# Kernel optimization log

Measured on AMD Instinct MI355X. Metric: run time of the kernel, lower is better.

## Reference

```python
import jax, jax.numpy as jnp
import numpy as np

N, D, H, C, E, I, L, B = 16000, 128, 2, 128, 256000, 512, 2, 64
NTYPES = 10


def setup_inputs() -> dict:
    key = jax.random.key(0)
    ks = jax.random.split(key, 20)
    s = 0.05
    inp = {
        'x': jax.random.normal(ks[0], (N, D), jnp.float32),
        'hetro_emb': jax.random.normal(ks[1], (NTYPES, D), jnp.float32) * s,
        'Wq': jax.random.normal(ks[2], (D, H * C), jnp.float32) * s,
        'bq': jnp.zeros((H * C,), jnp.float32),
        'Wk': jax.random.normal(ks[3], (D, H * C), jnp.float32) * s,
        'bk': jnp.zeros((H * C,), jnp.float32),
        'Wv': jax.random.normal(ks[4], (D, H * C), jnp.float32) * s,
        'bv': jnp.zeros((H * C,), jnp.float32),
        'We': jax.random.normal(ks[5], (D, H * C), jnp.float32) * s,
        'Wskip': jax.random.normal(ks[6], (D, C), jnp.float32) * s,
        'bskip': jnp.zeros((C,), jnp.float32),
        'ln_gamma': jnp.ones((L, D), jnp.float32),
        'ln_beta': jnp.zeros((L, D), jnp.float32),
        'ffn_w1': jax.random.normal(ks[7], (L, D, I), jnp.float32) * s,
        'ffn_b1': jnp.zeros((L, I), jnp.float32),
        'ffn_w2': jax.random.normal(ks[8], (L, I, D), jnp.float32) * s,
        'ffn_b2': jnp.zeros((L, D), jnp.float32),
        'edge_index': jax.random.randint(ks[9], (2, E), 0, N, jnp.int64),
        'edge_type': jax.random.randint(ks[10], (E,), 0, NTYPES, jnp.int64),
        'mask_idx': jax.random.randint(ks[11], (B,), 0, N, jnp.int64),
    }
    return inp


def _layer_norm(h, gamma, beta, eps=1e-6):
    mu = h.mean(-1, keepdims=True)
    var = ((h - mu) ** 2).mean(-1, keepdims=True)
    return (h - mu) * jax.lax.rsqrt(var + eps) * gamma + beta


def reference(x, hetro_emb, Wq, bq, Wk, bk, Wv, bv, We, Wskip, bskip,
              ln_gamma, ln_beta, ffn_w1, ffn_b1, ffn_w2, ffn_b2,
              edge_index, edge_type, mask_idx):
    src, dst = edge_index[0], edge_index[1]  # messages flow src(j) -> dst(i)
    edge_attr_raw = hetro_emb[edge_type]     # [E, D], computed once outside the layer loop
    scale = 1.0 / jnp.sqrt(jnp.asarray(C, x.dtype))

    h = x
    pre = h
    for l in range(L):
        # shared GRANConv weights across layers (same module appended n_gcn_layer times)
        q = (h @ Wq + bq).reshape(-1, H, C)
        k = (h @ Wk + bk).reshape(-1, H, C)
        v = (h @ Wv + bv).reshape(-1, H, C)
        eproj = (edge_attr_raw @ We).reshape(-1, H, C)  # [E, H, C]
        kj = k[src] + eproj                              # [E, H, C]
        logits = (q[dst] * kj).sum(-1) * scale           # [E, H]
        # segment softmax over destination nodes
        m = jax.ops.segment_max(logits, dst, num_segments=N)  # [N, H]
        a = jnp.exp(logits - m[dst])
        ssum = jax.ops.segment_sum(a, dst, num_segments=N)
        alpha = a / (ssum[dst] + 1e-16)                  # [E, H]
        msg = (v[src] + eproj) * alpha[..., None]        # [E, H, C]
        agg = jax.ops.segment_sum(msg, dst, num_segments=N)  # [N, H, C]
        out = agg.mean(1) + (h @ Wskip + bskip)          # concat=False -> head mean; root skip
        # residual + LN + FFN (no activation between the two FFN linears)
        hres = out + pre
        hln = _layer_norm(hres, ln_gamma[l], ln_beta[l])
        h = (hln @ ffn_w1[l] + ffn_b1[l]) @ ffn_w2[l] + ffn_b2[l]
        pre = h

    return h[mask_idx]  # [B, D]
```

## Files before the change

### kernel.cpp

```cpp
#include <hip/hip_runtime.h>
#include <hip/hip_bf16.h>
#include <math.h>

#define DD 128
#define QW 896
#define CAP 96

typedef _Float16 f16x8 __attribute__((ext_vector_type(8)));
typedef _Float16 f16x4 __attribute__((ext_vector_type(4)));
typedef float f32x4 __attribute__((ext_vector_type(4)));

__global__ __launch_bounds__(256) void count_kernel(const int* __restrict__ edst,
                                                    int* __restrict__ counts, int E) {
  int e = blockIdx.x * 256 + threadIdx.x;
  if (e < E) atomicAdd(&counts[edst[e]], 1);
}

__global__ __launch_bounds__(1024) void scan_kernel(const int* __restrict__ counts,
                                                    int* __restrict__ offs,
                                                    int* __restrict__ cursor, int Nn) {
  __shared__ int part[1024];
  int tid = threadIdx.x;
  int chunk = (Nn + 1023) >> 10;
  int b = tid * chunk, e = min(b + chunk, Nn);
  int s = 0;
  for (int j = b; j < e; ++j) s += counts[j];
  part[tid] = s;
  __syncthreads();
  for (int d = 1; d < 1024; d <<= 1) {
    int v = (tid >= d) ? part[tid - d] : 0;
    __syncthreads();
    part[tid] += v;
    __syncthreads();
  }
  int excl = tid ? part[tid - 1] : 0;
  for (int j = b; j < e; ++j) { offs[j] = excl; cursor[j] = excl; excl += counts[j]; }
  if (tid == 1023) offs[Nn] = part[1023];
}

__global__ __launch_bounds__(256) void scatter_kernel(const int* __restrict__ edst,
                                                      const int* __restrict__ esrc,
                                                      const int* __restrict__ etyp,
                                                      int* __restrict__ cursor,
                                                      unsigned* __restrict__ epk, int E) {
  int e = blockIdx.x * 256 + threadIdx.x;
  if (e < E) {
    int pos = atomicAdd(&cursor[edst[e]], 1);
    epk[pos] = (unsigned)esrc[e] | ((unsigned)etyp[e] << 18);
  }
}

__global__ __launch_bounds__(256) void precompute1(
    const float* __restrict__ Wq, const float* __restrict__ Wk,
    const float* __restrict__ Wv, const float* __restrict__ Wsk,
    const float* __restrict__ bq, const float* __restrict__ bk,
    const float* __restrict__ bv, const float* __restrict__ bsk,
    const float* __restrict__ hemb, const float* __restrict__ We,
    const float* __restrict__ x,
    const float* __restrict__ fw1, const float* __restrict__ fb1,
    const float* __restrict__ fw2, const float* __restrict__ fb2,
    _Float16* __restrict__ WcatT, float* __restrict__ Wcat, float* __restrict__ bcat,
    _Float16* __restrict__ epth, _Float16* __restrict__ xh,
    float* __restrict__ Wf, float* __restrict__ bfv, int Nn) {
  int t = blockIdx.x * 256 + threadIdx.x;
  if (t < 114688) {
    int n = t >> 7, k = t & 127;
    float v;
    if (n < 256) v = Wq[k * 256 + n];
    else if (n < 512) v = Wk[k * 256 + (n - 256)];
    else if (n < 768) v = Wv[k * 256 + (n - 512)];
    else v = Wsk[k * 128 + (n - 768)];
    WcatT[t] = (_Float16)v;
    Wcat[k * 896 + n] = v;
    return;
  }
  t -= 114688;
  if (t < 896) {
    float v;
    if (t < 256) v = bq[t];
    else if (t < 512) v = bk[t - 256];
    else if (t < 768) v = bv[t - 512];
    else v = bsk[t - 768];
    bcat[t] = v;
    return;
  }
  t -= 896;
  if (t < 2560) {
    int ty = t >> 8, col = t & 255;
    float s = 0.f;
#pragma unroll 4
    for (int c = 0; c < 128; ++c) s = fmaf(hemb[ty * 128 + c], We[c * 256 + col], s);
    epth[t] = (_Float16)s;
    return;
  }
  t -= 2560;
  if (t < Nn * 16) {
    float4 v0 = *reinterpret_cast<const float4*>(x + (size_t)t * 8);
    float4 v1 = *reinterpret_cast<const float4*>(x + (size_t)t * 8 + 4);
    f16x8 o;
    o[0] = (_Float16)v0.x; o[1] = (_Float16)v0.y; o[2] = (_Float16)v0.z; o[3] = (_Float16)v0.w;
    o[4] = (_Float16)v1.x; o[5] = (_Float16)v1.y; o[6] = (_Float16)v1.z; o[7] = (_Float16)v1.w;
    *reinterpret_cast<f16x8*>(xh + (size_t)t * 8) = o;
    return;
  }
  t -= Nn * 16;
  if (t < 32768) {
    int l = t >> 14, rem = t & 16383;
    int i2 = rem >> 7, j = rem & 127;
    const float* a = fw1 + (size_t)l * 65536 + i2 * 512;
    const float* b2 = fw2 + (size_t)l * 65536 + j;
    float s = 0.f;
#pragma unroll 4
    for (int k = 0; k < 512; ++k) s = fmaf(a[k], b2[k * 128], s);
    Wf[t] = s;
    return;
  }
  t -= 32768;
  if (t < 256) {
    int l = t >> 7, j = t & 127;
    const float* b1 = fb1 + l * 512;
    const float* w2 = fw2 + (size_t)l * 65536 + j;
    float s = fb2[l * 128 + j];
#pragma unroll 4
    for (int k = 0; k < 512; ++k) s = fmaf(b1[k], w2[k * 128], s);
    bfv[t] = s;
  }
}

__global__ __launch_bounds__(256) void precompute2(
    const float* __restrict__ Wf, const float* __restrict__ Wcat,
    const float* __restrict__ bfv, const float* __restrict__ bcat,
    _Float16* __restrict__ BtMid, float* __restrict__ bmid) {
  int t = blockIdx.x * 256 + threadIdx.x;
  if (t < 131072) {
    int k = t >> 10, n = t & 1023;
    float v;
    if (n < 128) v = Wf[k * 128 + n];
    else {
      const float* wr = Wf + k * 128;
      const float* wc = Wcat + (n - 128);
      float s = 0.f;
#pragma unroll 4
      for (int c = 0; c < 128; ++c) s = fmaf(wr[c], wc[c * 896], s);
      v = s;
    }
    BtMid[(size_t)n * 128 + k] = (_Float16)v;
    return;
  }
  t -= 131072;
  if (t < 1024) {
    float v;
    if (t < 128) v = bfv[t];
    else {
      const float* wc = Wcat + (t - 128);
      float s = bcat[t - 128];
#pragma unroll 4
      for (int c = 0; c < 128; ++c) s = fmaf(bfv[c], wc[c * 896], s);
      v = s;
    }
    bmid[t] = v;
  }
}

__global__ __launch_bounds__(256) void gemm_tn_f16(const _Float16* __restrict__ A,
                                                   const _Float16* __restrict__ Bt,
                                                   const float* __restrict__ bias,
                                                   float* __restrict__ Cf, int NF,
                                                   _Float16* __restrict__ Ch, int choff, int ldh,
                                                   int M, int N, int K) {
  const int tid = threadIdx.x;
  const int wid = tid >> 6, lane = tid & 63;
  const int wr = wid >> 1, wc = wid & 1;
  const int il = lane & 15, g = lane >> 4;
  const int row0 = blockIdx.x * 128 + wr * 64;
  const int col0 = blockIdx.y * 128 + wc * 64;
  const _Float16* Ap = A + (size_t)(row0 + il) * K + 8 * g;
  const _Float16* Bp = Bt + (size_t)(col0 + il) * K + 8 * g;
  f32x4 acc[4][4];
#pragma unroll
  for (int a = 0; a < 4; ++a)
#pragma unroll
    for (int b = 0; b < 4; ++b) acc[a][b] = (f32x4){0.f, 0.f, 0.f, 0.f};
  for (int k0 = 0; k0 < K; k0 += 32) {
    f16x8 af[4], bf[4];
#pragma unroll
    for (int f = 0; f < 4; ++f) {
      af[f] = *reinterpret_cast<const f16x8*>(Ap + (size_t)(f * 16) * K + k0);
      bf[f] = *reinterpret_cast<const f16x8*>(Bp + (size_t)(f * 16) * K + k0);
    }
#pragma unroll
    for (int fi = 0; fi < 4; ++fi)
#pragma unroll
      for (int fj = 0; fj < 4; ++fj)
        acc[fi][fj] = __builtin_amdgcn_mfma_f32_16x16x32_f16(af[fi], bf[fj], acc[fi][fj], 0, 0, 0);
  }
#pragma unroll
  for (int fj = 0; fj < 4; ++fj) {
    const int col = col0 + fj * 16 + il;
    const float b = bias[col];
#pragma unroll
    for (int fi = 0; fi < 4; ++fi) {
#pragma unroll
      for (int i = 0; i < 4; ++i) {
        const int row = row0 + fi * 16 + g * 4 + i;
        const float v = acc[fi][fj][i] + b;
        if (Cf && col < NF) Cf[(size_t)row * NF + col] = v;
        if (Ch && col >= choff) Ch[(size_t)row * ldh + (col - choff)] = (_Float16)v;
      }
    }
  }
}

__global__ __launch_bounds__(256) void node_attn_ln_kernel(
    const _Float16* __restrict__ QKVSh, const _Float16* __restrict__ epth,
    const float* __restrict__ hpre,
    const int* __restrict__ offs, const unsigned* __restrict__ epk,
    const float* __restrict__ gamma, const float* __restrict__ beta,
    _Float16* __restrict__ hlnh, int Nn) {
  __shared__ float sl0[4][CAP], sl1[4][CAP];
  __shared__ unsigned spk[4][CAP];
  __shared__ __align__(16) _Float16 elds[2560];
  const int tid = threadIdx.x;
  for (int t = tid; t < 1280; t += 256)
    reinterpret_cast<unsigned*>(elds)[t] = reinterpret_cast<const unsigned*>(epth)[t];
  __syncthreads();
  const int w = tid >> 6, lane = tid & 63;
  const int i = blockIdx.x * 4 + w;
  const int sub = lane >> 5;
  const int r = lane & 31;
  const int half = r >> 4;
  const int co = r << 3;
  const float scale = 0.08838834764831845f;
  float q[8];
  {
    f16x8 qv = *reinterpret_cast<const f16x8*>(QKVSh + (size_t)i * QW + co);
#pragma unroll
    for (int t = 0; t < 8; ++t) q[t] = (float)qv[t];
  }
  float m0 = -1e30f, m1 = -1e30f, s0 = 0.f, s1 = 0.f;
  float acc[8] = {0.f};
  const int ebeg = offs[i], eend = offs[i + 1];
  for (int cs = ebeg; cs < eend; cs += CAP) {
    const int cnt = min(CAP, eend - cs);
    for (int j = lane; j < cnt; j += 64) spk[w][j] = epk[cs + j];
    __threadfence_block();
    {
      int jj = (sub < cnt) ? sub : (cnt - 1);
      unsigned pk = spk[w][jj];
      f16x8 kv = *reinterpret_cast<const f16x8*>(QKVSh + (size_t)(pk & 0x3FFFF) * QW + 256 + co);
      f16x8 ev = *reinterpret_cast<const f16x8*>(elds + ((pk >> 18) << 8) + co);
      for (int j = 0; j < cnt; j += 2) {
        f16x8 kc = kv, ec = ev;
        const bool valid = (j + sub) < cnt;
        int jn = j + 2 + sub; if (jn > cnt - 1) jn = cnt - 1;
        pk = spk[w][jn];
        kv = *reinterpret_cast<const f16x8*>(QKVSh + (size_t)(pk & 0x3FFFF) * QW + 256 + co);
        ev = *reinterpret_cast<const f16x8*>(elds + ((pk >> 18) << 8) + co);
        float d = 0.f;
#pragma unroll
        for (int t = 0; t < 8; ++t) d = fmaf(q[t], (float)kc[t] + (float)ec[t], d);
        d += __shfl_xor(d, 1); d += __shfl_xor(d, 2);
        d += __shfl_xor(d, 4); d += __shfl_xor(d, 8);
        d *= scale;
        if (valid) {
          if (r == 0) sl0[w][j + sub] = d;
          if (r == 16) sl1[w][j + sub] = d;
        }
      }
    }
    __threadfence_block();
    float lm0 = -1e30f, lm1 = -1e30f;
    for (int j = lane; j < cnt; j += 64) {
      lm0 = fmaxf(lm0, sl0[w][j]); lm1 = fmaxf(lm1, sl1[w][j]);
    }
#pragma unroll
    for (int o = 32; o; o >>= 1) {
      lm0 = fmaxf(lm0, __shfl_xor(lm0, o)); lm1 = fmaxf(lm1, __shfl_xor(lm1, o));
    }
    const float nm0 = fmaxf(m0, lm0), nm1 = fmaxf(m1, lm1);
    const float r0 = __expf(m0 - nm0), r1 = __expf(m1 - nm1);
    const float rme = half ? r1 : r0;
    s0 *= r0; s1 *= r1;
#pragma unroll
    for (int t = 0; t < 8; ++t) acc[t] *= rme;
    m0 = nm0; m1 = nm1;
    float ls0 = 0.f, ls1 = 0.f;
    for (int j = lane; j < cnt; j += 64) {
      float e0 = __expf(sl0[w][j] - m0);
      float e1 = __expf(sl1[w][j] - m1);
      sl0[w][j] = e0; sl1[w][j] = e1;
      ls0 += e0; ls1 += e1;
    }
#pragma unroll
    for (int o = 32; o; o >>= 1) { ls0 += __shfl_xor(ls0, o); ls1 += __shfl_xor(ls1, o); }
    s0 += ls0; s1 += ls1;
    __threadfence_block();
    {
      int jj = (sub < cnt) ? sub : (cnt - 1);
      unsigned pk = spk[w][jj];
      f16x8 vv = *reinterpret_cast<const f16x8*>(QKVSh + (size_t)(pk & 0x3FFFF) * QW + 512 + co);
      f16x8 ev = *reinterpret_cast<const f16x8*>(elds + ((pk >> 18) << 8) + co);
      for (int j = 0; j < cnt; j += 2) {
        f16x8 vc = vv, ec = ev;
        const int jcur = j + sub;
        float wj = 0.f;
        if (jcur < cnt) wj = half ? sl1[w][jcur] : sl0[w][jcur];
        int jn = j + 2 + sub; if (jn > cnt - 1) jn = cnt - 1;
        pk = spk[w][jn];
        vv = *reinterpret_cast<const f16x8*>(QKVSh + (size_t)(pk & 0x3FFFF) * QW + 512 + co);
        ev = *reinterpret_cast<const f16x8*>(elds + ((pk >> 18) << 8) + co);
#pragma unroll
        for (int t = 0; t < 8; ++t) acc[t] = fmaf((float)vc[t] + (float)ec[t], wj, acc[t]);
      }
    }
  }
  const float inv0 = 1.f / (s0 + 1e-16f), inv1 = 1.f / (s1 + 1e-16f);
  const float invme = half ? inv1 : inv0;
  float g[8];
#pragma unroll
  for (int t = 0; t < 8; ++t) {
    float a = acc[t] + __shfl_xor(acc[t], 32);
    a *= invme;
    g[t] = 0.5f * (a + __shfl_xor(a, 16));
  }
  const int cm = (r & 15) << 3;
  f16x8 sk = *reinterpret_cast<const f16x8*>(QKVSh + (size_t)i * QW + 768 + cm);
  float4 p0 = *reinterpret_cast<const float4*>(hpre + (size_t)i * DD + cm);
  float4 p1 = *reinterpret_cast<const float4*>(hpre + (size_t)i * DD + cm + 4);
  float xv[8];
  xv[0] = g[0] + (float)sk[0] + p0.x; xv[1] = g[1] + (float)sk[1] + p0.y;
  xv[2] = g[2] + (float)sk[2] + p0.z; xv[3] = g[3] + (float)sk[3] + p0.w;
  xv[4] = g[4] + (float)sk[4] + p1.x; xv[5] = g[5] + (float)sk[5] + p1.y;
  xv[6] = g[6] + (float)sk[6] + p1.z; xv[7] = g[7] + (float)sk[7] + p1.w;
  float sm = 0.f;
#pragma unroll
  for (int t = 0; t < 8; ++t) sm += xv[t];
  sm += __shfl_xor(sm, 1); sm += __shfl_xor(sm, 2);
  sm += __shfl_xor(sm, 4); sm += __shfl_xor(sm, 8);
  const float mu = sm * (1.f / 128.f);
  float vvs = 0.f;
  float dx[8];
#pragma unroll
  for (int t = 0; t < 8; ++t) { dx[t] = xv[t] - mu; vvs += dx[t] * dx[t]; }
  vvs += __shfl_xor(vvs, 1); vvs += __shfl_xor(vvs, 2);
  vvs += __shfl_xor(vvs, 4); vvs += __shfl_xor(vvs, 8);
  const float rstd = rsqrtf(vvs * (1.f / 128.f) + 1e-6f);
  if (lane < 16) {
    float4 gm0 = *reinterpret_cast<const float4*>(gamma + cm);
    float4 gm1 = *reinterpret_cast<const float4*>(gamma + cm + 4);
    float4 bt0 = *reinterpret_cast<const float4*>(beta + cm);
    float4 bt1 = *reinterpret_cast<const float4*>(beta + cm + 4);
    f16x8 o;
    o[0] = (_Float16)(dx[0] * rstd * gm0.x + bt0.x);
    o[1] = (_Float16)(dx[1] * rstd * gm0.y + bt0.y);
    o[2] = (_Float16)(dx[2] * rstd * gm0.z + bt0.z);
    o[3] = (_Float16)(dx[3] * rstd * gm0.w + bt0.w);
    o[4] = (_Float16)(dx[4] * rstd * gm1.x + bt1.x);
    o[5] = (_Float16)(dx[5] * rstd * gm1.y + bt1.y);
    o[6] = (_Float16)(dx[6] * rstd * gm1.z + bt1.z);
    o[7] = (_Float16)(dx[7] * rstd * gm1.w + bt1.w);
    *reinterpret_cast<f16x8*>(hlnh + (size_t)i * DD + cm) = o;
  }
}

__global__ __launch_bounds__(128) void final_kernel(const _Float16* __restrict__ hlnh1,
                                                    const float* __restrict__ Wf,
                                                    const float* __restrict__ bfv,
                                                    const int* __restrict__ midx,
                                                    float* __restrict__ out) {
  __shared__ float rowv[128];
  const int b = blockIdx.x, j = threadIdx.x;
  const int row = midx[b];
  rowv[j] = (float)hlnh1[(size_t)row * DD + j];
  __syncthreads();
  const float* w1 = Wf + 16384 + j;
  float s = bfv[128 + j];
#pragma unroll 4
  for (int c = 0; c < 128; ++c) s = fmaf(rowv[c], w1[c * 128], s);
  out[b * DD + j] = s;
}

extern "C" void kernel_launch(void* const* d_in, const int* in_sizes, int n_in,
                              void* d_out, int out_size, void* d_ws, size_t ws_size,
                              hipStream_t stream) {
  const float* x    = (const float*)d_in[0];
  const float* hemb = (const float*)d_in[1];
  const float* Wq   = (const float*)d_in[2];
  const float* bq   = (const float*)d_in[3];
  const float* Wk   = (const float*)d_in[4];
  const float* bk   = (const float*)d_in[5];
  const float* Wv   = (const float*)d_in[6];
  const float* bv   = (const float*)d_in[7];
  const float* We   = (const float*)d_in[8];
  const float* Wsk  = (const float*)d_in[9];
  const float* bsk  = (const float*)d_in[10];
  const float* lng  = (const float*)d_in[11];
  const float* lnb  = (const float*)d_in[12];
  const float* fw1  = (const float*)d_in[13];
  const float* fb1  = (const float*)d_in[14];
  const float* fw2  = (const float*)d_in[15];
  const float* fb2  = (const float*)d_in[16];
  const int* eidx   = (const int*)d_in[17];
  const int* etyp   = (const int*)d_in[18];
  const int* midx   = (const int*)d_in[19];

  const int Nn = in_sizes[0] / DD;
  const int E = in_sizes[18];

  const int* esrc = eidx;
  const int* edst = eidx + E;

  char* p = (char*)d_ws;
  auto alloc = [&](size_t bytes) -> void* {
    void* r = (void*)p;
    p += (bytes + 255) & ~(size_t)255;
    return r;
  };
  _Float16* QKVSh = (_Float16*)alloc((size_t)Nn * QW * 2);
  _Float16* xh    = (_Float16*)alloc((size_t)Nn * DD * 2);
  _Float16* hln0  = (_Float16*)alloc((size_t)Nn * DD * 2);
  _Float16* hln1  = (_Float16*)alloc((size_t)Nn * DD * 2);
  float*    h1    = (float*)alloc((size_t)Nn * DD * 4);
  _Float16* WcatT = (_Float16*)alloc((size_t)QW * DD * 2);
  float*    Wcat  = (float*)alloc((size_t)DD * QW * 4);
  float*    bcat  = (float*)alloc(QW * 4);
  _Float16* epth  = (_Float16*)alloc(2560 * 2);
  float*    Wf    = (float*)alloc(2 * 128 * 128 * 4);
  float*    bfv   = (float*)alloc(256 * 4);
  _Float16* BtMid = (_Float16*)alloc((size_t)1024 * 128 * 2);
  float*    bmid  = (float*)alloc(1024 * 4);
  int* counts = (int*)alloc((size_t)Nn * 4);
  int* offs   = (int*)alloc((size_t)(Nn + 1) * 4);
  int* cursor = (int*)alloc((size_t)Nn * 4);
  unsigned* epk = (unsigned*)alloc((size_t)E * 4);

  hipMemsetAsync(counts, 0, (size_t)Nn * sizeof(int), stream);
  count_kernel<<<(E + 255) / 256, 256, 0, stream>>>(edst, counts, E);
  scan_kernel<<<1, 1024, 0, stream>>>(counts, offs, cursor, Nn);
  scatter_kernel<<<(E + 255) / 256, 256, 0, stream>>>(edst, esrc, etyp, cursor, epk, E);

  const int p1_threads = 114688 + 896 + 2560 + Nn * 16 + 32768 + 256;
  precompute1<<<(p1_threads + 255) / 256, 256, 0, stream>>>(
      Wq, Wk, Wv, Wsk, bq, bk, bv, bsk, hemb, We, x, fw1, fb1, fw2, fb2,
      WcatT, Wcat, bcat, epth, xh, Wf, bfv, Nn);
  precompute2<<<(131072 + 1024 + 255) / 256, 256, 0, stream>>>(Wf, Wcat, bfv, bcat, BtMid, bmid);

  dim3 g1(Nn / 128, QW / 128);
  gemm_tn_f16<<<g1, 256, 0, stream>>>(xh, WcatT, bcat, nullptr, 0, QKVSh, 0, QW, Nn, QW, DD);
  node_attn_ln_kernel<<<Nn / 4, 256, 0, stream>>>(QKVSh, epth, x, offs, epk,
                                                  lng, lnb, hln0, Nn);
  dim3 g2(Nn / 128, 1024 / 128);
  gemm_tn_f16<<<g2, 256, 0, stream>>>(hln0, BtMid, bmid, h1, 128, QKVSh, 128, QW, Nn, 1024, DD);
  node_attn_ln_kernel<<<Nn / 4, 256, 0, stream>>>(QKVSh, epth, h1, offs, epk,
                                                  lng + DD, lnb + DD, hln1, Nn);
  final_kernel<<<64, 128, 0, stream>>>(hln1, Wf, bfv, midx, (float*)d_out);
}
```

Before: 280.9 us.

## Compute fused FFN weights via MFMA GEMMs and restructure edge attention

```diff
diff --git a/kernel.cpp b/kernel.cpp
--- a/kernel.cpp
+++ b/kernel.cpp
@@ -4,11 +4,20 @@
 
 #define DD 128
 #define QW 896
-#define CAP 96
+#define CAP 128
 
 typedef _Float16 f16x8 __attribute__((ext_vector_type(8)));
 typedef _Float16 f16x4 __attribute__((ext_vector_type(4)));
+typedef _Float16 f16x2 __attribute__((ext_vector_type(2)));
 typedef float f32x4 __attribute__((ext_vector_type(4)));
+
+__device__ __forceinline__ float fdot2f(f16x2 a, f16x2 b, float c) {
+#if __has_builtin(__builtin_amdgcn_fdot2)
+  return __builtin_amdgcn_fdot2(a, b, c, false);
+#else
+  return fmaf((float)a[0], (float)b[0], fmaf((float)a[1], (float)b[1], c));
+#endif
+}
 
 __global__ __launch_bounds__(256) void count_kernel(const int* __restrict__ edst,
                                                     int* __restrict__ counts, int E) {
@@ -50,7 +59,7 @@
   }
 }
 
-__global__ __launch_bounds__(256) void precompute1(
+__global__ __launch_bounds__(256) void pp_cast(
     const float* __restrict__ Wq, const float* __restrict__ Wk,
     const float* __restrict__ Wv, const float* __restrict__ Wsk,
     const float* __restrict__ bq, const float* __restrict__ bk,
@@ -61,8 +70,38 @@
     const float* __restrict__ fw2, const float* __restrict__ fb2,
     _Float16* __restrict__ WcatT, float* __restrict__ Wcat, float* __restrict__ bcat,
     _Float16* __restrict__ epth, _Float16* __restrict__ xh,
-    float* __restrict__ Wf, float* __restrict__ bfv, int Nn) {
+    _Float16* __restrict__ fw1h, _Float16* __restrict__ fw2Th,
+    float* __restrict__ bfv, float* __restrict__ bzero, int Nn) {
   int t = blockIdx.x * 256 + threadIdx.x;
+  if (t < 256) {
+    int l = t >> 7, j = t & 127;
+    const float* b1 = fb1 + l * 512;
+    const float* w2 = fw2 + (size_t)l * 65536 + j;
+    float s0 = fb2[l * 128 + j], s1 = 0.f, s2 = 0.f, s3 = 0.f;
+    for (int k = 0; k < 512; k += 4) {
+      s0 = fmaf(b1[k], w2[(size_t)k * 128], s0);
+      s1 = fmaf(b1[k + 1], w2[(size_t)(k + 1) * 128], s1);
+      s2 = fmaf(b1[k + 2], w2[(size_t)(k + 2) * 128], s2);
+      s3 = fmaf(b1[k + 3], w2[(size_t)(k + 3) * 128], s3);
+    }
+    bfv[t] = ((s0 + s1) + (s2 + s3));
+    return;
+  }
+  t -= 256;
+  if (t < 2560) {
+    int ty = t >> 8, col = t & 255;
+    float s0 = 0.f, s1 = 0.f, s2 = 0.f, s3 = 0.f;
+    const float* hr = hemb + ty * 128;
+    for (int c = 0; c < 128; c += 4) {
+      s0 = fmaf(hr[c], We[c * 256 + col], s0);
+      s1 = fmaf(hr[c + 1], We[(c + 1) * 256 + col], s1);
+      s2 = fmaf(hr[c + 2], We[(c + 2) * 256 + col], s2);
+      s3 = fmaf(hr[c + 3], We[(c + 3) * 256 + col], s3);
+    }
+    epth[t] = (_Float16)((s0 + s1) + (s2 + s3));
+    return;
+  }
+  t -= 2560;
   if (t < 114688) {
     int n = t >> 7, k = t & 127;
     float v;
@@ -85,15 +124,25 @@
     return;
   }
   t -= 896;
-  if (t < 2560) {
-    int ty = t >> 8, col = t & 255;
-    float s = 0.f;
-#pragma unroll 4
-    for (int c = 0; c < 128; ++c) s = fmaf(hemb[ty * 128 + c], We[c * 256 + col], s);
-    epth[t] = (_Float16)s;
-    return;
-  }
-  t -= 2560;
+  if (t < 1024) { bzero[t] = 0.f; return; }
+  t -= 1024;
+  if (t < 16384) {
+    float4 v0 = *reinterpret_cast<const float4*>(fw1 + (size_t)t * 8);
+    float4 v1 = *reinterpret_cast<const float4*>(fw1 + (size_t)t * 8 + 4);
+    f16x8 o;
+    o[0] = (_Float16)v0.x; o[1] = (_Float16)v0.y; o[2] = (_Float16)v0.z; o[3] = (_Float16)v0.w;
+    o[4] = (_Float16)v1.x; o[5] = (_Float16)v1.y; o[6] = (_Float16)v1.z; o[7] = (_Float16)v1.w;
+    *reinterpret_cast<f16x8*>(fw1h + (size_t)t * 8) = o;
+    return;
+  }
+  t -= 16384;
+  if (t < 131072) {
+    int l = t >> 16, rem = t & 65535;
+    int j = rem >> 9, k = rem & 511;
+    fw2Th[t] = (_Float16)fw2[(size_t)l * 65536 + (size_t)k * 128 + j];
+    return;
+  }
+  t -= 131072;
   if (t < Nn * 16) {
     float4 v0 = *reinterpret_cast<const float4*>(x + (size_t)t * 8);
     float4 v1 = *reinterpret_cast<const float4*>(x + (size_t)t * 8 + 4);
@@ -101,65 +150,25 @@
     o[0] = (_Float16)v0.x; o[1] = (_Float16)v0.y; o[2] = (_Float16)v0.z; o[3] = (_Float16)v0.w;
     o[4] = (_Float16)v1.x; o[5] = (_Float16)v1.y; o[6] = (_Float16)v1.z; o[7] = (_Float16)v1.w;
     *reinterpret_cast<f16x8*>(xh + (size_t)t * 8) = o;
-    return;
-  }
-  t -= Nn * 16;
-  if (t < 32768) {
-    int l = t >> 14, rem = t & 16383;
-    int i2 = rem >> 7, j = rem & 127;
-    const float* a = fw1 + (size_t)l * 65536 + i2 * 512;
-    const float* b2 = fw2 + (size_t)l * 65536 + j;
-    float s = 0.f;
-#pragma unroll 4
-    for (int k = 0; k < 512; ++k) s = fmaf(a[k], b2[k * 128], s);
-    Wf[t] = s;
-    return;
-  }
-  t -= 32768;
-  if (t < 256) {
-    int l = t >> 7, j = t & 127;
-    const float* b1 = fb1 + l * 512;
-    const float* w2 = fw2 + (size_t)l * 65536 + j;
-    float s = fb2[l * 128 + j];
-#pragma unroll 4
-    for (int k = 0; k < 512; ++k) s = fmaf(b1[k], w2[k * 128], s);
-    bfv[t] = s;
-  }
-}
-
-__global__ __launch_bounds__(256) void precompute2(
-    const float* __restrict__ Wf, const float* __restrict__ Wcat,
-    const float* __restrict__ bfv, const float* __restrict__ bcat,
-    _Float16* __restrict__ BtMid, float* __restrict__ bmid) {
+  }
+}
+
+__global__ __launch_bounds__(256) void pp_bmid(const float* __restrict__ bfv,
+                                               const float* __restrict__ Wcat,
+                                               const float* __restrict__ bcat,
+                                               float* __restrict__ bmid) {
   int t = blockIdx.x * 256 + threadIdx.x;
-  if (t < 131072) {
-    int k = t >> 10, n = t & 1023;
-    float v;
-    if (n < 128) v = Wf[k * 128 + n];
-    else {
-      const float* wr = Wf + k * 128;
-      const float* wc = Wcat + (n - 128);
-      float s = 0.f;
-#pragma unroll 4
-      for (int c = 0; c < 128; ++c) s = fmaf(wr[c], wc[c * 896], s);
-      v = s;
-    }
-    BtMid[(size_t)n * 128 + k] = (_Float16)v;
-    return;
-  }
-  t -= 131072;
-  if (t < 1024) {
-    float v;
-    if (t < 128) v = bfv[t];
-    else {
-      const float* wc = Wcat + (t - 128);
-      float s = bcat[t - 128];
-#pragma unroll 4
-      for (int c = 0; c < 128; ++c) s = fmaf(bfv[c], wc[c * 896], s);
-      v = s;
-    }
-    bmid[t] = v;
-  }
+  if (t >= 1024) return;
+  if (t < 128) { bmid[t] = bfv[t]; return; }
+  int n = t - 128;
+  float s0 = bcat[n], s1 = 0.f, s2 = 0.f, s3 = 0.f;
+  for (int c = 0; c < 128; c += 4) {
+    s0 = fmaf(bfv[c], Wcat[c * 896 + n], s0);
+    s1 = fmaf(bfv[c + 1], Wcat[(c + 1) * 896 + n], s1);
+    s2 = fmaf(bfv[c + 2], Wcat[(c + 2) * 896 + n], s2);
+    s3 = fmaf(bfv[c + 3], Wcat[(c + 3) * 896 + n], s3);
+  }
+  bmid[t] = ((s0 + s1) + (s2 + s3));
 }
 
 __global__ __launch_bounds__(256) void gemm_tn_f16(const _Float16* __restrict__ A,
@@ -167,6 +176,7 @@
                                                    const float* __restrict__ bias,
                                                    float* __restrict__ Cf, int NF,
                                                    _Float16* __restrict__ Ch, int choff, int ldh,
+                                                   _Float16* __restrict__ ChT, int ldt,
                                                    int M, int N, int K) {
   const int tid = threadIdx.x;
   const int wid = tid >> 6, lane = tid & 63;
@@ -174,6 +184,8 @@
   const int il = lane & 15, g = lane >> 4;
   const int row0 = blockIdx.x * 128 + wr * 64;
   const int col0 = blockIdx.y * 128 + wc * 64;
+  const bool arow_ok = (row0 + il + 48) < M || true;
+  (void)arow_ok;
   const _Float16* Ap = A + (size_t)(row0 + il) * K + 8 * g;
   const _Float16* Bp = Bt + (size_t)(col0 + il) * K + 8 * g;
   f32x4 acc[4][4];
@@ -185,7 +197,8 @@
     f16x8 af[4], bf[4];
 #pragma unroll
     for (int f = 0; f < 4; ++f) {
-      af[f] = *reinterpret_cast<const f16x8*>(Ap + (size_t)(f * 16) * K + k0);
+      af[f] = (row0 + f * 16 + il) < M ? *reinterpret_cast<const f16x8*>(Ap + (size_t)(f * 16) * K + k0)
+                                       : (f16x8){0, 0, 0, 0, 0, 0, 0, 0};
       bf[f] = *reinterpret_cast<const f16x8*>(Bp + (size_t)(f * 16) * K + k0);
     }
 #pragma unroll
@@ -203,9 +216,11 @@
 #pragma unroll
       for (int i = 0; i < 4; ++i) {
         const int row = row0 + fi * 16 + g * 4 + i;
+        if (row >= M) continue;
         const float v = acc[fi][fj][i] + b;
         if (Cf && col < NF) Cf[(size_t)row * NF + col] = v;
         if (Ch && col >= choff) Ch[(size_t)row * ldh + (col - choff)] = (_Float16)v;
+        if (ChT) ChT[(size_t)col * ldt + row] = (_Float16)v;
       }
     }
   }
@@ -217,8 +232,9 @@
     const int* __restrict__ offs, const unsigned* __restrict__ epk,
     const float* __restrict__ gamma, const float* __restrict__ beta,
     _Float16* __restrict__ hlnh, int Nn) {
-  __shared__ float sl0[4][CAP], sl1[4][CAP];
+  __shared__ float slA[4][CAP], slB[4][CAP];
   __shared__ unsigned spk[4][CAP];
+  __shared__ float stA[4][10], stB[4][10];
   __shared__ __align__(16) _Float16 elds[2560];
   const int tid = threadIdx.x;
   for (int t = tid; t < 1280; t += 256)
@@ -226,16 +242,14 @@
   __syncthreads();
   const int w = tid >> 6, lane = tid & 63;
   const int i = blockIdx.x * 4 + w;
-  const int sub = lane >> 5;
-  const int r = lane & 31;
-  const int half = r >> 4;
-  const int co = r << 3;
+  const int et = lane >> 2, cl = lane & 3, cbase = cl << 6;
+  const int sub = lane >> 5, r = lane & 31, half = r >> 4, co = r << 3;
   const float scale = 0.08838834764831845f;
-  float q[8];
+  f16x8 q8[8];
   {
-    f16x8 qv = *reinterpret_cast<const f16x8*>(QKVSh + (size_t)i * QW + co);
-#pragma unroll
-    for (int t = 0; t < 8; ++t) q[t] = (float)qv[t];
+    const _Float16* qp = QKVSh + (size_t)i * QW + cbase;
+#pragma unroll
+    for (int c = 0; c < 8; ++c) q8[c] = *reinterpret_cast<const f16x8*>(qp + c * 8);
   }
   float m0 = -1e30f, m1 = -1e30f, s0 = 0.f, s1 = 0.f;
   float acc[8] = {0.f};
@@ -243,75 +257,83 @@
   for (int cs = ebeg; cs < eend; cs += CAP) {
     const int cnt = min(CAP, eend - cs);
     for (int j = lane; j < cnt; j += 64) spk[w][j] = epk[cs + j];
+    if (lane < 10) { stA[w][lane] = 0.f; stB[w][lane] = 0.f; }
     __threadfence_block();
-    {
-      int jj = (sub < cnt) ? sub : (cnt - 1);
-      unsigned pk = spk[w][jj];
-      f16x8 kv = *reinterpret_cast<const f16x8*>(QKVSh + (size_t)(pk & 0x3FFFF) * QW + 256 + co);
-      f16x8 ev = *reinterpret_cast<const f16x8*>(elds + ((pk >> 18) << 8) + co);
-      for (int j = 0; j < cnt; j += 2) {
-        f16x8 kc = kv, ec = ev;
-        const bool valid = (j + sub) < cnt;
-        int jn = j + 2 + sub; if (jn > cnt - 1) jn = cnt - 1;
-        pk = spk[w][jn];
-        kv = *reinterpret_cast<const f16x8*>(QKVSh + (size_t)(pk & 0x3FFFF) * QW + 256 + co);
-        ev = *reinterpret_cast<const f16x8*>(elds + ((pk >> 18) << 8) + co);
-        float d = 0.f;
-#pragma unroll
-        for (int t = 0; t < 8; ++t) d = fmaf(q[t], (float)kc[t] + (float)ec[t], d);
-        d += __shfl_xor(d, 1); d += __shfl_xor(d, 2);
-        d += __shfl_xor(d, 4); d += __shfl_xor(d, 8);
-        d *= scale;
-        if (valid) {
-          if (r == 0) sl0[w][j + sub] = d;
-          if (r == 16) sl1[w][j + sub] = d;
-        }
+    float tmax = -1e30f;
+    for (int j0 = 0; j0 < cnt; j0 += 16) {
+      const int j = j0 + et;
+      const bool valid = j < cnt;
+      const unsigned pk = spk[w][valid ? j : cnt - 1];
+      const _Float16* kp = QKVSh + (size_t)(pk & 0x3FFFF) * QW + 256 + cbase;
+      const _Float16* ep = elds + ((pk >> 18) << 8) + cbase;
+      f16x8 kv[8];
+#pragma unroll
+      for (int c = 0; c < 8; ++c) kv[c] = *reinterpret_cast<const f16x8*>(kp + c * 8);
+      float d = 0.f;
+#pragma unroll
+      for (int c = 0; c < 8; ++c) {
+        f16x8 sum = kv[c] + *reinterpret_cast<const f16x8*>(ep + c * 8);
+        const f16x2* sp = reinterpret_cast<const f16x2*>(&sum);
+        const f16x2* qp2 = reinterpret_cast<const f16x2*>(&q8[c]);
+#pragma unroll
+        for (int p2 = 0; p2 < 4; ++p2) d = fdot2f(qp2[p2], sp[p2], d);
       }
-    }
-    __threadfence_block();
-    float lm0 = -1e30f, lm1 = -1e30f;
-    for (int j = lane; j < cnt; j += 64) {
-      lm0 = fmaxf(lm0, sl0[w][j]); lm1 = fmaxf(lm1, sl1[w][j]);
-    }
-#pragma unroll
-    for (int o = 32; o; o >>= 1) {
-      lm0 = fmaxf(lm0, __shfl_xor(lm0, o)); lm1 = fmaxf(lm1, __shfl_xor(lm1, o));
-    }
-    const float nm0 = fmaxf(m0, lm0), nm1 = fmaxf(m1, lm1);
+      d += __shfl_xor(d, 1);
+      d *= scale;
+      if (valid) {
+        if (cl == 0) slA[w][j] = d;
+        else if (cl == 2) slB[w][j] = d;
+        tmax = fmaxf(tmax, d);
+      }
+    }
+#pragma unroll
+    for (int o = 4; o <= 32; o <<= 1) tmax = fmaxf(tmax, __shfl_xor(tmax, o));
+    const float tOther = __shfl_xor(tmax, 2);
+    const float cm0 = (lane & 2) ? tOther : tmax;
+    const float cm1 = (lane & 2) ? tmax : tOther;
+    const float nm0 = fmaxf(m0, cm0), nm1 = fmaxf(m1, cm1);
     const float r0 = __expf(m0 - nm0), r1 = __expf(m1 - nm1);
     const float rme = half ? r1 : r0;
     s0 *= r0; s1 *= r1;
 #pragma unroll
     for (int t = 0; t < 8; ++t) acc[t] *= rme;
     m0 = nm0; m1 = nm1;
+    __threadfence_block();
     float ls0 = 0.f, ls1 = 0.f;
     for (int j = lane; j < cnt; j += 64) {
-      float e0 = __expf(sl0[w][j] - m0);
-      float e1 = __expf(sl1[w][j] - m1);
-      sl0[w][j] = e0; sl1[w][j] = e1;
+      float e0 = __expf(slA[w][j] - m0);
+      float e1 = __expf(slB[w][j] - m1);
+      slA[w][j] = e0; slB[w][j] = e1;
       ls0 += e0; ls1 += e1;
+      int ty = spk[w][j] >> 18;
+      atomicAdd(&stA[w][ty], e0);
+      atomicAdd(&stB[w][ty], e1);
     }
 #pragma unroll
     for (int o = 32; o; o >>= 1) { ls0 += __shfl_xor(ls0, o); ls1 += __shfl_xor(ls1, o); }
     s0 += ls0; s1 += ls1;
     __threadfence_block();
     {
-      int jj = (sub < cnt) ? sub : (cnt - 1);
-      unsigned pk = spk[w][jj];
-      f16x8 vv = *reinterpret_cast<const f16x8*>(QKVSh + (size_t)(pk & 0x3FFFF) * QW + 512 + co);
-      f16x8 ev = *reinterpret_cast<const f16x8*>(elds + ((pk >> 18) << 8) + co);
+      f16x8 v0 = *reinterpret_cast<const f16x8*>(
+          QKVSh + (size_t)(spk[w][min(sub, cnt - 1)] & 0x3FFFF) * QW + 512 + co);
+      f16x8 v1 = *reinterpret_cast<const f16x8*>(
+          QKVSh + (size_t)(spk[w][min(2 + sub, cnt - 1)] & 0x3FFFF) * QW + 512 + co);
       for (int j = 0; j < cnt; j += 2) {
-        f16x8 vc = vv, ec = ev;
-        const int jcur = j + sub;
-        float wj = 0.f;
-        if (jcur < cnt) wj = half ? sl1[w][jcur] : sl0[w][jcur];
-        int jn = j + 2 + sub; if (jn > cnt - 1) jn = cnt - 1;
-        pk = spk[w][jn];
-        vv = *reinterpret_cast<const f16x8*>(QKVSh + (size_t)(pk & 0x3FFFF) * QW + 512 + co);
-        ev = *reinterpret_cast<const f16x8*>(elds + ((pk >> 18) << 8) + co);
-#pragma unroll
-        for (int t = 0; t < 8; ++t) acc[t] = fmaf((float)vc[t] + (float)ec[t], wj, acc[t]);
+        f16x8 cur = v0; v0 = v1;
+        v1 = *reinterpret_cast<const f16x8*>(
+            QKVSh + (size_t)(spk[w][min(j + 4 + sub, cnt - 1)] & 0x3FFFF) * QW + 512 + co);
+        const int jj = j + sub;
+        const float wj = (jj < cnt) ? (half ? slB[w][jj] : slA[w][jj]) : 0.f;
+#pragma unroll
+        for (int t = 0; t < 8; ++t) acc[t] = fmaf((float)cur[t], wj, acc[t]);
       }
+    }
+#pragma unroll
+    for (int ty = 0; ty < 10; ++ty) {
+      const float a = half ? stB[w][ty] : stA[w][ty];
+      f16x8 ev = *reinterpret_cast<const f16x8*>(elds + (ty << 8) + co);
+#pragma unroll
+      for (int t = 0; t < 8; ++t) acc[t] = fmaf((float)ev[t], a, acc[t]);
     }
   }
   const float inv0 = 1.f / (s0 + 1e-16f), inv1 = 1.f / (s1 + 1e-16f);
@@ -338,8 +360,7 @@
   sm += __shfl_xor(sm, 1); sm += __shfl_xor(sm, 2);
   sm += __shfl_xor(sm, 4); sm += __shfl_xor(sm, 8);
   const float mu = sm * (1.f / 128.f);
-  float vvs = 0.f;
-  float dx[8];
+  float dx[8], vvs = 0.f;
 #pragma unroll
   for (int t = 0; t < 8; ++t) { dx[t] = xv[t] - mu; vvs += dx[t] * dx[t]; }
   vvs += __shfl_xor(vvs, 1); vvs += __shfl_xor(vvs, 2);
@@ -425,8 +446,12 @@
   float*    Wcat  = (float*)alloc((size_t)DD * QW * 4);
   float*    bcat  = (float*)alloc(QW * 4);
   _Float16* epth  = (_Float16*)alloc(2560 * 2);
+  _Float16* fw1h  = (_Float16*)alloc((size_t)2 * DD * 512 * 2);
+  _Float16* fw2Th = (_Float16*)alloc((size_t)2 * DD * 512 * 2);
   float*    Wf    = (float*)alloc(2 * 128 * 128 * 4);
+  _Float16* Wfh   = (_Float16*)alloc(128 * 128 * 2);
   float*    bfv   = (float*)alloc(256 * 4);
+  float*    bzero = (float*)alloc(1024 * 4);
   _Float16* BtMid = (_Float16*)alloc((size_t)1024 * 128 * 2);
   float*    bmid  = (float*)alloc(1024 * 4);
   int* counts = (int*)alloc((size_t)Nn * 4);
@@ -439,18 +464,29 @@
   scan_kernel<<<1, 1024, 0, stream>>>(counts, offs, cursor, Nn);
   scatter_kernel<<<(E + 255) / 256, 256, 0, stream>>>(edst, esrc, etyp, cursor, epk, E);
 
-  const int p1_threads = 114688 + 896 + 2560 + Nn * 16 + 32768 + 256;
-  precompute1<<<(p1_threads + 255) / 256, 256, 0, stream>>>(
+  const int pc_threads = 256 + 2560 + 114688 + 896 + 1024 + 16384 + 131072 + Nn * 16;
+  pp_cast<<<(pc_threads + 255) / 256, 256, 0, stream>>>(
       Wq, Wk, Wv, Wsk, bq, bk, bv, bsk, hemb, We, x, fw1, fb1, fw2, fb2,
-      WcatT, Wcat, bcat, epth, xh, Wf, bfv, Nn);
-  precompute2<<<(131072 + 1024 + 255) / 256, 256, 0, stream>>>(Wf, Wcat, bfv, bcat, BtMid, bmid);
-
-  dim3 g1(Nn / 128, QW / 128);
-  gemm_tn_f16<<<g1, 256, 0, stream>>>(xh, WcatT, bcat, nullptr, 0, QKVSh, 0, QW, Nn, QW, DD);
+      WcatT, Wcat, bcat, epth, xh, fw1h, fw2Th, bfv, bzero, Nn);
+  pp_bmid<<<4, 256, 0, stream>>>(bfv, Wcat, bcat, bmid);
+  gemm_tn_f16<<<dim3(1, 1), 256, 0, stream>>>(fw1h, fw2Th, bzero,
+                                              Wf, 128, Wfh, 0, 128, BtMid, 128,
+                                              128, 128, 512);
+  gemm_tn_f16<<<dim3(1, 1), 256, 0, stream>>>(fw1h + 65536, fw2Th + 65536, bzero,
+                                              Wf + 16384, 128, nullptr, 0, 0, nullptr, 0,
+                                              128, 128, 512);
+  gemm_tn_f16<<<dim3(1, 7), 256, 0, stream>>>(Wfh, WcatT, bzero,
+                                              nullptr, 0, nullptr, 0, 0, BtMid + 16384, 128,
+                                              128, 896, 128);
+
+  dim3 g1((Nn + 127) / 128, QW / 128);
+  gemm_tn_f16<<<g1, 256, 0, stream>>>(xh, WcatT, bcat, nullptr, 0, QKVSh, 0, QW,
+                                      nullptr, 0, Nn, QW, DD);
   node_attn_ln_kernel<<<Nn / 4, 256, 0, stream>>>(QKVSh, epth, x, offs, epk,
                                                   lng, lnb, hln0, Nn);
-  dim3 g2(Nn / 128, 1024 / 128);
-  gemm_tn_f16<<<g2, 256, 0, stream>>>(hln0, BtMid, bmid, h1, 128, QKVSh, 128, QW, Nn, 1024, DD);
+  dim3 g2((Nn + 127) / 128, 1024 / 128);
+  gemm_tn_f16<<<g2, 256, 0, stream>>>(hln0, BtMid, bmid, h1, 128, QKVSh, 128, QW,
+                                      nullptr, 0, Nn, 1024, DD);
   node_attn_ln_kernel<<<Nn / 4, 256, 0, stream>>>(QKVSh, epth, h1, offs, epk,
                                                   lng + DD, lnb + DD, hln1, Nn);
   final_kernel<<<64, 128, 0, stream>>>(hln1, Wf, bfv, midx, (float*)d_out);
```

Result: slower. 406.9 us (+44.9%).
